# Performance work log

Hardware: AMD Instinct MI355X
Metric: run time of the kernel (lower is better)

Reference implementation:

```python
import jax, jax.numpy as jnp
import numpy as np

NEG_BIG = -9.0e15  # matches -9000000000000000.0 in the torch source


def setup_inputs() -> dict:
    key = jax.random.key(0)
    k1, k2 = jax.random.split(key)
    N, D, L = 8192, 128, 2
    features = jax.random.normal(k1, (N, D), dtype=jnp.float32)
    adj_lst = jax.random.randint(k2, (L, N, N), 0, 2, dtype=jnp.int32)
    return {"features": features, "adj_lst": adj_lst}


def reference(features, adj_lst):
    # features: [N, D] float; adj_lst: [L, N, N] int (0/1)
    n_node = features.shape[0]
    for i in range(adj_lst.shape[0]):  # small fixed number of propagation steps
        adj = adj_lst[i]
        mask = adj > 0
        # raw_weight = ones -> masked logits are 1.0 on edges, -9e15 elsewhere
        logits = jnp.where(mask, jnp.float32(1.0), jnp.float32(NEG_BIG))
        attention = jax.nn.softmax(logits, axis=1)          # [N, N] row-stochastic
        prop_fea = attention @ features                     # [N, D] neighbor mean
        adj_num = jnp.sum(adj, axis=1)                      # degree per node
        adj_mask = (adj_num > 0).astype(features.dtype)[:, None]  # [N, 1]
        features = adj_mask * prop_fea + (1.0 - adj_mask) * features
    return features
```

## Files before the change

kernel.cpp:

```cpp
#include <hip/hip_runtime.h>
#include <hip/hip_bf16.h>

typedef __bf16 bf16x8 __attribute__((ext_vector_type(8)));
typedef float f32x4 __attribute__((ext_vector_type(4)));
typedef float f32x16 __attribute__((ext_vector_type(16)));
typedef int int4v __attribute__((ext_vector_type(4)));
typedef unsigned int uint4v __attribute__((ext_vector_type(4)));
typedef unsigned short u16x8 __attribute__((ext_vector_type(8)));

#define N_NODES 8192
#define D_FEAT 128


__device__ __forceinline__ bf16x8 unpack_byte(unsigned dword, int sh) {
  unsigned P = ((dword >> sh) & 0xFFu) * 0x8001u;
  uint4v c;
  c[0] = (P & 0x10001u) * 0x3F80u;
  c[1] = ((P >> 2) & 0x10001u) * 0x3F80u;
  c[2] = ((P >> 4) & 0x10001u) * 0x3F80u;
  c[3] = ((P >> 6) & 0x10001u) * 0x3F80u;
  return __builtin_bit_cast(bf16x8, c);
}

__device__ __forceinline__ void bpk32_store(const float* __restrict__ src,
                                            unsigned short* __restrict__ Bpk,
                                            int W) {
  const int kk = W >> 8;
  const int ng = (W >> 6) & 3;
  const int l = W & 63;
  const int d = ng * 32 + (l & 31);
  const int p0 = kk * 16 + (l >> 5) * 8;
  const int n0 = (p0 >> 8) * 256 + ((p0 >> 3) & 7) * 32 + ((p0 >> 6) & 3);
  u16x8 pk;
#pragma unroll
  for (int e = 0; e < 8; ++e) {
    __bf16 v = (__bf16)src[(long)(n0 + 4 * e) * D_FEAT + d];
    pk[e] = __builtin_bit_cast(unsigned short, v);
  }
  *(u16x8*)(Bpk + (long)W * 8) = pk;
}

__global__ __launch_bounds__(256) void bpk_build32_kernel(
    const float* __restrict__ src, unsigned short* __restrict__ Bpk) {
  bpk32_store(src, Bpk, blockIdx.x * 256 + threadIdx.x);
}

__global__ __launch_bounds__(512, 2) void fused_layer_kernel(
    const int* __restrict__ adj, const unsigned short* __restrict__ Bpk,
    const float* __restrict__ fin, float* __restrict__ fout) {
  __shared__ unsigned bitsL[2][320];
  __shared__ int degL[32];
  __shared__ __align__(16) f32x4 red[4][4][64];

  const int tid = threadIdx.x;
  const int lane = tid & 63;
  const int w = tid >> 6;
  const int ng = w & 3;
  const int kh2 = w >> 2;
  const int l31 = lane & 31;
  const int lh = lane >> 5;
  const int lh8 = lh * 8;
  const int m0 = blockIdx.x * 32;

  const int4v* aB0 = (const int4v*)(adj + ((long)(m0 + w) << 13)) + lane;
  const int4v* aB1 = (const int4v*)(adj + ((long)(m0 + 8 + w) << 13)) + lane;
  const int4v* aB2 = (const int4v*)(adj + ((long)(m0 + 16 + w) << 13)) + lane;
  const int4v* aB3 = (const int4v*)(adj + ((long)(m0 + 24 + w) << 13)) + lane;

  int cnt0 = 0, cnt1 = 0, cnt2 = 0, cnt3 = 0;

#define DO_BALLOT(R0, R1, R2, R3, BUF)                                       \
  {                                                                          \
    const int e_ = lane >> 1;                                                \
    _Pragma("unroll") for (int i = 0; i < 4; ++i) {                          \
      int4v vv = (i == 0) ? (R0) : (i == 1) ? (R1) : (i == 2) ? (R2) : (R3); \
      unsigned long long b0 = __ballot(vv[0] != 0);                          \
      unsigned long long b1 = __ballot(vv[1] != 0);                          \
      unsigned long long b2 = __ballot(vv[2] != 0);                          \
      unsigned long long b3 = __ballot(vv[3] != 0);                          \
      int pc = __popcll(b0) + __popcll(b1) + __popcll(b2) + __popcll(b3);    \
      if (i == 0) cnt0 += pc;                                                \
      if (i == 1) cnt1 += pc;                                                \
      if (i == 2) cnt2 += pc;                                                \
      if (i == 3) cnt3 += pc;                                                \
      unsigned long long bsel = b0;                                          \
      if (e_ == 1) bsel = b1;                                                \
      if (e_ == 2) bsel = b2;                                                \
      if (e_ == 3) bsel = b3;                                                \
      unsigned dv = (lane & 1) ? (unsigned)(bsel >> 32) : (unsigned)bsel;    \
      if (lane < 8) bitsL[BUF][(i * 8 + w) * 10 + lane] = dv;                \
    }                                                                        \
  }

  f32x16 acc = {0.f, 0.f, 0.f, 0.f, 0.f, 0.f, 0.f, 0.f,
                0.f, 0.f, 0.f, 0.f, 0.f, 0.f, 0.f, 0.f};

#define DO_GEMM(C, BUF)                                                      \
  {                                                                          \
    const bf16x8* bp = (const bf16x8*)Bpk +                                  \
                       (((long)((C)*16 + kh2 * 8)) << 8) + ng * 64 + lane;   \
    bf16x8 bv0 = bp[0], bv1 = bp[256], bv2 = bp[512], bv3 = bp[768];         \
    bf16x8 bv4 = bp[1024], bv5 = bp[1280], bv6 = bp[1536], bv7 = bp[1792];   \
    const unsigned* bl = &bitsL[BUF][l31 * 10 + kh2 * 4];                    \
    unsigned q0 = bl[0], q1 = bl[1], q2 = bl[2], q3 = bl[3];                 \
    acc = __builtin_amdgcn_mfma_f32_32x32x16_bf16(unpack_byte(q0, lh8),      \
                                                  bv0, acc, 0, 0, 0);        \
    acc = __builtin_amdgcn_mfma_f32_32x32x16_bf16(unpack_byte(q0, lh8 + 16), \
                                                  bv1, acc, 0, 0, 0);        \
    acc = __builtin_amdgcn_mfma_f32_32x32x16_bf16(unpack_byte(q1, lh8),      \
                                                  bv2, acc, 0, 0, 0);        \
    acc = __builtin_amdgcn_mfma_f32_32x32x16_bf16(unpack_byte(q1, lh8 + 16), \
                                                  bv3, acc, 0, 0, 0);        \
    acc = __builtin_amdgcn_mfma_f32_32x32x16_bf16(unpack_byte(q2, lh8),      \
                                                  bv4, acc, 0, 0, 0);        \
    acc = __builtin_amdgcn_mfma_f32_32x32x16_bf16(unpack_byte(q2, lh8 + 16), \
                                                  bv5, acc, 0, 0, 0);        \
    acc = __builtin_amdgcn_mfma_f32_32x32x16_bf16(unpack_byte(q3, lh8),      \
                                                  bv6, acc, 0, 0, 0);        \
    acc = __builtin_amdgcn_mfma_f32_32x32x16_bf16(unpack_byte(q3, lh8 + 16), \
                                                  bv7, acc, 0, 0, 0);        \
  }

  int4v avA0 = aB0[0], avA1 = aB1[0], avA2 = aB2[0], avA3 = aB3[0];
  int4v avB0 = aB0[64], avB1 = aB1[64], avB2 = aB2[64], avB3 = aB3[64];
  DO_BALLOT(avA0, avA1, avA2, avA3, 0)
  __syncthreads();

#define BODY(C, CUR0, CUR1, CUR2, CUR3, OTH0, OTH1, OTH2, OTH3)              \
  {                                                                          \
    if ((C) + 2 < 32) {                                                      \
      CUR0 = aB0[((C) + 2) * 64];                                            \
      CUR1 = aB1[((C) + 2) * 64];                                            \
      CUR2 = aB2[((C) + 2) * 64];                                            \
      CUR3 = aB3[((C) + 2) * 64];                                            \
    }                                                                        \
    if ((C) + 1 < 32) DO_BALLOT(OTH0, OTH1, OTH2, OTH3, ((C) + 1) & 1)       \
    DO_GEMM((C), (C)&1)                                                      \
    __syncthreads();                                                         \
  }

  for (int c = 0; c < 32; c += 2) {
    BODY(c, avA0, avA1, avA2, avA3, avB0, avB1, avB2, avB3)
    BODY(c + 1, avB0, avB1, avB2, avB3, avA0, avA1, avA2, avA3)
  }
#undef BODY
#undef DO_GEMM
#undef DO_BALLOT

  if (lane == 0) {
    degL[w] = cnt0;
    degL[8 + w] = cnt1;
    degL[16 + w] = cnt2;
    degL[24 + w] = cnt3;
  }

  if (kh2) {
#define ST4(c)                                                               \
  red[ng][c][lane] = __builtin_shufflevector(acc, acc, 4 * (c), 4 * (c) + 1, \
                                             4 * (c) + 2, 4 * (c) + 3);
    ST4(0) ST4(1) ST4(2) ST4(3)
#undef ST4
  }
  __syncthreads();
  if (kh2) return;
#pragma unroll
  for (int c = 0; c < 4; ++c) {
    f32x4 r = red[ng][c][lane];
#pragma unroll
    for (int k = 0; k < 4; ++k) acc[4 * c + k] += r[k];
  }

#pragma unroll
  for (int r = 0; r < 16; ++r) {
    const int row32 = (r & 3) + 8 * (r >> 2) + 4 * lh;
    const int row = m0 + row32;
    const int dg = degL[row32];
    const long off = (long)row * D_FEAT + ng * 32 + l31;
    fout[off] = dg > 0 ? acc[r] * (1.0f / (float)dg) : fin[off];
  }
}

__global__ __launch_bounds__(256) void transpose_cast_kernel(
    const float* __restrict__ src, unsigned short* __restrict__ dst) {
  __shared__ float tile[64][129];
  const int t = threadIdx.x;
  const int nbase = blockIdx.x * 64;
#pragma unroll
  for (int i = 0; i < 32; ++i) {
    int idx = t + i * 256;
    int nl = idx >> 7;
    int d = idx & 127;
    tile[nl][d] = src[(long)(nbase + nl) * D_FEAT + d];
  }
  __syncthreads();
#pragma unroll
  for (int i = 0; i < 32; ++i) {
    int idx = t + i * 256;
    int d = idx >> 6;
    int nl = idx & 63;
    __bf16 b = (__bf16)tile[nl][d];
    dst[(long)d * N_NODES + nbase + nl] = __builtin_bit_cast(unsigned short, b);
  }
}

__global__ __launch_bounds__(512) void layer_kernel_direct(
    const int* __restrict__ adj, const unsigned short* __restrict__ BT,
    const float* __restrict__ fin, float* __restrict__ fout) {
  const int tid = threadIdx.x;
  const int lane = tid & 63;
  const int w = tid >> 6;
  const int m0 = blockIdx.x * 32 + (w >> 2) * 16;
  const int n0 = (w & 3) * 32;
  const int lr = lane & 15;
  const int kc = lane >> 4;

  const int4v* ap = (const int4v*)(adj + (long)(m0 + lr) * N_NODES + kc * 8);
  const bf16x8* bp0 = (const bf16x8*)(BT + (long)(n0 + lr) * N_NODES + kc * 8);
  const bf16x8* bp1 =
      (const bf16x8*)(BT + (long)(n0 + 16 + lr) * N_NODES + kc * 8);

  f32x4 acc0 = {0.f, 0.f, 0.f, 0.f};
  f32x4 acc1 = {0.f, 0.f, 0.f, 0.f};
  int degv = 0;

#pragma unroll 4
  for (int k = 0; k < N_NODES; k += 32) {
    int4v alo = ap[0];
    int4v ahi = ap[1];
    bf16x8 b0 = bp0[0];
    bf16x8 b1 = bp1[0];
    ap += 8;
    bp0 += 4;
    bp1 += 4;
    unsigned short u[8];
    u[0] = alo[0] ? 0x3F80 : 0;
    u[1] = alo[1] ? 0x3F80 : 0;
    u[2] = alo[2] ? 0x3F80 : 0;
    u[3] = alo[3] ? 0x3F80 : 0;
    u[4] = ahi[0] ? 0x3F80 : 0;
    u[5] = ahi[1] ? 0x3F80 : 0;
    u[6] = ahi[2] ? 0x3F80 : 0;
    u[7] = ahi[3] ? 0x3F80 : 0;
    degv += alo[0] + alo[1] + alo[2] + alo[3] + ahi[0] + ahi[1] + ahi[2] +
            ahi[3];
    bf16x8 a;
    memcpy(&a, u, 16);
    acc0 = __builtin_amdgcn_mfma_f32_16x16x32_bf16(a, b0, acc0, 0, 0, 0);
    acc1 = __builtin_amdgcn_mfma_f32_16x16x32_bf16(a, b1, acc1, 0, 0, 0);
  }

  degv += __shfl_xor(degv, 16);
  degv += __shfl_xor(degv, 32);
  int dgv[4];
#pragma unroll
  for (int j = 0; j < 4; ++j) dgv[j] = __shfl(degv, kc * 4 + j);

#pragma unroll
  for (int t = 0; t < 2; ++t) {
    const f32x4 acc = t ? acc1 : acc0;
    const int col = n0 + t * 16 + lr;
#pragma unroll
    for (int j = 0; j < 4; ++j) {
      const long off = (long)(m0 + kc * 4 + j) * D_FEAT + col;
      fout[off] = dgv[j] > 0 ? acc[j] * (1.0f / (float)dgv[j]) : fin[off];
    }
  }
}

extern "C" void kernel_launch(void* const* d_in, const int* in_sizes, int n_in,
                              void* d_out, int out_size, void* d_ws,
                              size_t ws_size, hipStream_t stream) {
  const float* features = (const float*)d_in[0];
  const int* adj = (const int*)d_in[1];
  float* out = (float*)d_out;
  const long NN = (long)N_NODES * N_NODES;

  const size_t BPK_BYTES = (size_t)D_FEAT * N_NODES * 2;
  const size_t NEED = BPK_BYTES + 256;

  if (ws_size >= NEED) {
    unsigned short* Bpk = (unsigned short*)d_ws;

    bpk_build32_kernel<<<512, 256, 0, stream>>>(features, Bpk);
    fused_layer_kernel<<<256, 512, 0, stream>>>(adj, Bpk, features, out);
    bpk_build32_kernel<<<512, 256, 0, stream>>>(out, Bpk);
    fused_layer_kernel<<<256, 512, 0, stream>>>(adj + NN, Bpk, out, out);
  } else {
    unsigned short* BTw = (unsigned short*)d_ws;
    transpose_cast_kernel<<<N_NODES / 64, 256, 0, stream>>>(features, BTw);
    layer_kernel_direct<<<N_NODES / 32, 512, 0, stream>>>(adj, BTw, features,
                                                          out);
    transpose_cast_kernel<<<N_NODES / 64, 256, 0, stream>>>(out, BTw);
    layer_kernel_direct<<<N_NODES / 32, 512, 0, stream>>>(adj + NN, BTw, out,
                                                          out);
  }
}
```

Baseline: 157.6 us.

## Split-K adjacency GEMM with 128-row tiles, XCD-aware mapping, and combine pass

Each layer's main kernel now handles a 128-row by quarter-K tile instead of 32 rows over the full K. Each wave processes 16 adjacency rows and computes two 32x32 accumulators, so each loaded B fragment feeds two MFMAs. Block indices are remapped so blocks on the same XCD share a K quarter, which should improve L2 reuse of the packed features. Partial sums and degrees go to workspace and a new combine kernel reduces them, adding extra global traffic, a launch per layer and a larger workspace requirement.

```diff
diff --git a/kernel.cpp b/kernel.cpp
--- a/kernel.cpp
+++ b/kernel.cpp
@@ -45,139 +45,151 @@
   bpk32_store(src, Bpk, blockIdx.x * 256 + threadIdx.x);
 }
 
-__global__ __launch_bounds__(512, 2) void fused_layer_kernel(
+__global__ __launch_bounds__(512, 2) void fused_split_kernel(
     const int* __restrict__ adj, const unsigned short* __restrict__ Bpk,
-    const float* __restrict__ fin, float* __restrict__ fout) {
-  __shared__ unsigned bitsL[2][320];
-  __shared__ int degL[32];
-  __shared__ __align__(16) f32x4 red[4][4][64];
+    float* __restrict__ pC, unsigned short* __restrict__ degP) {
+  __shared__ unsigned bitsL[2][1536];
 
   const int tid = threadIdx.x;
   const int lane = tid & 63;
   const int w = tid >> 6;
-  const int ng = w & 3;
-  const int kh2 = w >> 2;
   const int l31 = lane & 31;
   const int lh = lane >> 5;
   const int lh8 = lh * 8;
-  const int m0 = blockIdx.x * 32;
-
-  const int4v* aB0 = (const int4v*)(adj + ((long)(m0 + w) << 13)) + lane;
-  const int4v* aB1 = (const int4v*)(adj + ((long)(m0 + 8 + w) << 13)) + lane;
-  const int4v* aB2 = (const int4v*)(adj + ((long)(m0 + 16 + w) << 13)) + lane;
-  const int4v* aB3 = (const int4v*)(adj + ((long)(m0 + 24 + w) << 13)) + lane;
-
-  int cnt0 = 0, cnt1 = 0, cnt2 = 0, cnt3 = 0;
-
-#define DO_BALLOT(R0, R1, R2, R3, BUF)                                       \
+  const int mh = w >> 2;
+  const int ng = w & 3;
+
+  const int bx = blockIdx.x;
+  const int xcd = bx & 7;
+  const int kq = xcd >> 1;
+  const int rowblk = (bx >> 3) + ((xcd & 1) << 5);
+  const int m0 = rowblk * 128;
+
+  const int* aR = adj + ((long)(m0 + w * 16) << 13) + (long)kq * 2048;
+
+  int4v av[16];
+  int cnt[16];
+#pragma unroll
+  for (int i = 0; i < 16; ++i) cnt[i] = 0;
+
+  f32x16 accA = {0.f, 0.f, 0.f, 0.f, 0.f, 0.f, 0.f, 0.f,
+                 0.f, 0.f, 0.f, 0.f, 0.f, 0.f, 0.f, 0.f};
+  f32x16 accB = accA;
+
+#define LOAD_CHUNK(C)                                                        \
+  {                                                                          \
+    _Pragma("unroll") for (int i = 0; i < 16; ++i)                           \
+        av[i] = *((const int4v*)(aR + ((long)i << 13)) + (C)*64 + lane);     \
+  }
+
+#define DO_BALLOT(BUF)                                                       \
   {                                                                          \
     const int e_ = lane >> 1;                                                \
-    _Pragma("unroll") for (int i = 0; i < 4; ++i) {                          \
-      int4v vv = (i == 0) ? (R0) : (i == 1) ? (R1) : (i == 2) ? (R2) : (R3); \
-      unsigned long long b0 = __ballot(vv[0] != 0);                          \
-      unsigned long long b1 = __ballot(vv[1] != 0);                          \
-      unsigned long long b2 = __ballot(vv[2] != 0);                          \
-      unsigned long long b3 = __ballot(vv[3] != 0);                          \
-      int pc = __popcll(b0) + __popcll(b1) + __popcll(b2) + __popcll(b3);    \
-      if (i == 0) cnt0 += pc;                                                \
-      if (i == 1) cnt1 += pc;                                                \
-      if (i == 2) cnt2 += pc;                                                \
-      if (i == 3) cnt3 += pc;                                                \
+    _Pragma("unroll") for (int i = 0; i < 16; ++i) {                         \
+      unsigned long long b0 = __ballot(av[i][0] != 0);                       \
+      unsigned long long b1 = __ballot(av[i][1] != 0);                       \
+      unsigned long long b2 = __ballot(av[i][2] != 0);                       \
+      unsigned long long b3 = __ballot(av[i][3] != 0);                       \
+      cnt[i] += __popcll(b0) + __popcll(b1) + __popcll(b2) + __popcll(b3);   \
       unsigned long long bsel = b0;                                          \
       if (e_ == 1) bsel = b1;                                                \
       if (e_ == 2) bsel = b2;                                                \
       if (e_ == 3) bsel = b3;                                                \
       unsigned dv = (lane & 1) ? (unsigned)(bsel >> 32) : (unsigned)bsel;    \
-      if (lane < 8) bitsL[BUF][(i * 8 + w) * 10 + lane] = dv;                \
+      if (lane < 8) bitsL[BUF][(w * 16 + i) * 12 + lane] = dv;               \
     }                                                                        \
   }
 
-  f32x16 acc = {0.f, 0.f, 0.f, 0.f, 0.f, 0.f, 0.f, 0.f,
-                0.f, 0.f, 0.f, 0.f, 0.f, 0.f, 0.f, 0.f};
-
-#define DO_GEMM(C, BUF)                                                      \
+#define GEMM_HALF(C, BUF, KH2)                                               \
   {                                                                          \
     const bf16x8* bp = (const bf16x8*)Bpk +                                  \
-                       (((long)((C)*16 + kh2 * 8)) << 8) + ng * 64 + lane;   \
+        (((long)((kq * 8 + (C)) * 16 + (KH2)*8)) << 8) + ng * 64 + lane;     \
     bf16x8 bv0 = bp[0], bv1 = bp[256], bv2 = bp[512], bv3 = bp[768];         \
     bf16x8 bv4 = bp[1024], bv5 = bp[1280], bv6 = bp[1536], bv7 = bp[1792];   \
-    const unsigned* bl = &bitsL[BUF][l31 * 10 + kh2 * 4];                    \
-    unsigned q0 = bl[0], q1 = bl[1], q2 = bl[2], q3 = bl[3];                 \
-    acc = __builtin_amdgcn_mfma_f32_32x32x16_bf16(unpack_byte(q0, lh8),      \
-                                                  bv0, acc, 0, 0, 0);        \
-    acc = __builtin_amdgcn_mfma_f32_32x32x16_bf16(unpack_byte(q0, lh8 + 16), \
-                                                  bv1, acc, 0, 0, 0);        \
-    acc = __builtin_amdgcn_mfma_f32_32x32x16_bf16(unpack_byte(q1, lh8),      \
-                                                  bv2, acc, 0, 0, 0);        \
-    acc = __builtin_amdgcn_mfma_f32_32x32x16_bf16(unpack_byte(q1, lh8 + 16), \
-                                                  bv3, acc, 0, 0, 0);        \
-    acc = __builtin_amdgcn_mfma_f32_32x32x16_bf16(unpack_byte(q2, lh8),      \
-                                                  bv4, acc, 0, 0, 0);        \
-    acc = __builtin_amdgcn_mfma_f32_32x32x16_bf16(unpack_byte(q2, lh8 + 16), \
-                                                  bv5, acc, 0, 0, 0);        \
-    acc = __builtin_amdgcn_mfma_f32_32x32x16_bf16(unpack_byte(q3, lh8),      \
-                                                  bv6, acc, 0, 0, 0);        \
-    acc = __builtin_amdgcn_mfma_f32_32x32x16_bf16(unpack_byte(q3, lh8 + 16), \
-                                                  bv7, acc, 0, 0, 0);        \
-  }
-
-  int4v avA0 = aB0[0], avA1 = aB1[0], avA2 = aB2[0], avA3 = aB3[0];
-  int4v avB0 = aB0[64], avB1 = aB1[64], avB2 = aB2[64], avB3 = aB3[64];
-  DO_BALLOT(avA0, avA1, avA2, avA3, 0)
+    const uint4v* bq = (const uint4v*)(&bitsL[BUF][0]);                      \
+    uint4v qA = bq[(mh * 64 + l31) * 3 + (KH2)];                             \
+    uint4v qB = bq[(mh * 64 + 32 + l31) * 3 + (KH2)];                        \
+    accA = __builtin_amdgcn_mfma_f32_32x32x16_bf16(unpack_byte(qA[0], lh8),  \
+                                                   bv0, accA, 0, 0, 0);      \
+    accB = __builtin_amdgcn_mfma_f32_32x32x16_bf16(unpack_byte(qB[0], lh8),  \
+                                                   bv0, accB, 0, 0, 0);      \
+    accA = __builtin_amdgcn_mfma_f32_32x32x16_bf16(                          \
+        unpack_byte(qA[0], lh8 + 16), bv1, accA, 0, 0, 0);                   \
+    accB = __builtin_amdgcn_mfma_f32_32x32x16_bf16(                          \
+        unpack_byte(qB[0], lh8 + 16), bv1, accB, 0, 0, 0);                   \
+    accA = __builtin_amdgcn_mfma_f32_32x32x16_bf16(unpack_byte(qA[1], lh8),  \
+                                                   bv2, accA, 0, 0, 0);      \
+    accB = __builtin_amdgcn_mfma_f32_32x32x16_bf16(unpack_byte(qB[1], lh8),  \
+                                                   bv2, accB, 0, 0, 0);      \
+    accA = __builtin_amdgcn_mfma_f32_32x32x16_bf16(                          \
+        unpack_byte(qA[1], lh8 + 16), bv3, accA, 0, 0, 0);                   \
+    accB = __builtin_amdgcn_mfma_f32_32x32x16_bf16(                          \
+        unpack_byte(qB[1], lh8 + 16), bv3, accB, 0, 0, 0);                   \
+    accA = __builtin_amdgcn_mfma_f32_32x32x16_bf16(unpack_byte(qA[2], lh8),  \
+                                                   bv4, accA, 0, 0, 0);      \
+    accB = __builtin_amdgcn_mfma_f32_32x32x16_bf16(unpack_byte(qB[2], lh8),  \
+                                                   bv4, accB, 0, 0, 0);      \
+    accA = __builtin_amdgcn_mfma_f32_32x32x16_bf16(                          \
+        unpack_byte(qA[2], lh8 + 16), bv5, accA, 0, 0, 0);                   \
+    accB = __builtin_amdgcn_mfma_f32_32x32x16_bf16(                          \
+        unpack_byte(qB[2], lh8 + 16), bv5, accB, 0, 0, 0);                   \
+    accA = __builtin_amdgcn_mfma_f32_32x32x16_bf16(unpack_byte(qA[3], lh8),  \
+                                                   bv6, accA, 0, 0, 0);      \
+    accB = __builtin_amdgcn_mfma_f32_32x32x16_bf16(unpack_byte(qB[3], lh8),  \
+                                                   bv6, accB, 0, 0, 0);      \
+    accA = __builtin_amdgcn_mfma_f32_32x32x16_bf16(                          \
+        unpack_byte(qA[3], lh8 + 16), bv7, accA, 0, 0, 0);                   \
+    accB = __builtin_amdgcn_mfma_f32_32x32x16_bf16(                          \
+        unpack_byte(qB[3], lh8 + 16), bv7, accB, 0, 0, 0);                   \
+  }
+
+  LOAD_CHUNK(0)
+  DO_BALLOT(0)
+  LOAD_CHUNK(1)
   __syncthreads();
 
-#define BODY(C, CUR0, CUR1, CUR2, CUR3, OTH0, OTH1, OTH2, OTH3)              \
-  {                                                                          \
-    if ((C) + 2 < 32) {                                                      \
-      CUR0 = aB0[((C) + 2) * 64];                                            \
-      CUR1 = aB1[((C) + 2) * 64];                                            \
-      CUR2 = aB2[((C) + 2) * 64];                                            \
-      CUR3 = aB3[((C) + 2) * 64];                                            \
-    }                                                                        \
-    if ((C) + 1 < 32) DO_BALLOT(OTH0, OTH1, OTH2, OTH3, ((C) + 1) & 1)       \
-    DO_GEMM((C), (C)&1)                                                      \
-    __syncthreads();                                                         \
-  }
-
-  for (int c = 0; c < 32; c += 2) {
-    BODY(c, avA0, avA1, avA2, avA3, avB0, avB1, avB2, avB3)
-    BODY(c + 1, avB0, avB1, avB2, avB3, avA0, avA1, avA2, avA3)
-  }
-#undef BODY
-#undef DO_GEMM
+  for (int c = 0; c < 8; ++c) {
+    if (c + 1 < 8) DO_BALLOT((c + 1) & 1)
+    if (c + 2 < 8) LOAD_CHUNK(c + 2)
+    GEMM_HALF(c, c & 1, 0)
+    GEMM_HALF(c, c & 1, 1)
+    __syncthreads();
+  }
+#undef GEMM_HALF
 #undef DO_BALLOT
+#undef LOAD_CHUNK
 
   if (lane == 0) {
-    degL[w] = cnt0;
-    degL[8 + w] = cnt1;
-    degL[16 + w] = cnt2;
-    degL[24 + w] = cnt3;
-  }
-
-  if (kh2) {
-#define ST4(c)                                                               \
-  red[ng][c][lane] = __builtin_shufflevector(acc, acc, 4 * (c), 4 * (c) + 1, \
-                                             4 * (c) + 2, 4 * (c) + 3);
-    ST4(0) ST4(1) ST4(2) ST4(3)
-#undef ST4
-  }
-  __syncthreads();
-  if (kh2) return;
-#pragma unroll
-  for (int c = 0; c < 4; ++c) {
-    f32x4 r = red[ng][c][lane];
-#pragma unroll
-    for (int k = 0; k < 4; ++k) acc[4 * c + k] += r[k];
-  }
-
+#pragma unroll
+    for (int i = 0; i < 16; ++i)
+      degP[kq * N_NODES + m0 + w * 16 + i] = (unsigned short)cnt[i];
+  }
+
+  float* base = pC + ((long)kq << 20);
 #pragma unroll
   for (int r = 0; r < 16; ++r) {
-    const int row32 = (r & 3) + 8 * (r >> 2) + 4 * lh;
-    const int row = m0 + row32;
-    const int dg = degL[row32];
-    const long off = (long)row * D_FEAT + ng * 32 + l31;
-    fout[off] = dg > 0 ? acc[r] * (1.0f / (float)dg) : fin[off];
-  }
+    const int rr = (r & 3) + 8 * (r >> 2) + 4 * lh;
+    base[(long)(m0 + mh * 64 + rr) * D_FEAT + ng * 32 + l31] = accA[r];
+    base[(long)(m0 + mh * 64 + 32 + rr) * D_FEAT + ng * 32 + l31] = accB[r];
+  }
+}
+
+__global__ __launch_bounds__(256) void combine_kernel(
+    const float* __restrict__ pC, const unsigned short* __restrict__ degP,
+    const float* __restrict__ fin, float* __restrict__ fout) {
+  const int g = blockIdx.x * 256 + threadIdx.x;
+  const int row = g >> 5;
+  const f32x4* P = (const f32x4*)pC;
+  f32x4 s = P[g] + P[262144 + g] + P[524288 + g] + P[786432 + g];
+  const int dg = (int)degP[row] + degP[N_NODES + row] + degP[2 * N_NODES + row] +
+                 degP[3 * N_NODES + row];
+  f32x4 o;
+  if (dg > 0) {
+    o = s * (1.0f / (float)dg);
+  } else {
+    o = ((const f32x4*)fin)[g];
+  }
+  ((f32x4*)fout)[g] = o;
 }
 
 __global__ __launch_bounds__(256) void transpose_cast_kernel(
@@ -275,16 +287,23 @@
   float* out = (float*)d_out;
   const long NN = (long)N_NODES * N_NODES;
 
+  const size_t PC_BYTES = 4ul * N_NODES * D_FEAT * 4;
+  const size_t DEG_BYTES = 4ul * N_NODES * 2;
   const size_t BPK_BYTES = (size_t)D_FEAT * N_NODES * 2;
-  const size_t NEED = BPK_BYTES + 256;
+  const size_t NEED = PC_BYTES + DEG_BYTES + BPK_BYTES;
 
   if (ws_size >= NEED) {
-    unsigned short* Bpk = (unsigned short*)d_ws;
+    float* pC = (float*)d_ws;
+    unsigned short* degP = (unsigned short*)((char*)d_ws + PC_BYTES);
+    unsigned short* Bpk =
+        (unsigned short*)((char*)d_ws + PC_BYTES + DEG_BYTES);
 
     bpk_build32_kernel<<<512, 256, 0, stream>>>(features, Bpk);
-    fused_layer_kernel<<<256, 512, 0, stream>>>(adj, Bpk, features, out);
+    fused_split_kernel<<<256, 512, 0, stream>>>(adj, Bpk, pC, degP);
+    combine_kernel<<<1024, 256, 0, stream>>>(pC, degP, features, out);
     bpk_build32_kernel<<<512, 256, 0, stream>>>(out, Bpk);
-    fused_layer_kernel<<<256, 512, 0, stream>>>(adj + NN, Bpk, out, out);
+    fused_split_kernel<<<256, 512, 0, stream>>>(adj + NN, Bpk, pC, degP);
+    combine_kernel<<<1024, 256, 0, stream>>>(pC, degP, out, out);
   } else {
     unsigned short* BTw = (unsigned short*)d_ws;
     transpose_cast_kernel<<<N_NODES / 64, 256, 0, stream>>>(features, BTw);
```

Result: slower. 171.7 us (+9.0%).

## Split the reduction dimension across two blocks and add a combine kernel

Applied to the files above, without the earlier changes.

Each layer's fused kernel now runs 512 blocks, and each block handles half of the K (neighbor) range for a 32-row tile. The partial sums and partial degree counts go to workspace, and a new combine kernel adds them, normalizes by degree, or falls back to the input features. The goal is more blocks than the 256-CU device so the memory-bound adjacency stream keeps more CUs busy. The cost is an extra kernel launch per layer, plus the traffic to write and reread the partial results.

```diff
diff --git a/kernel.cpp b/kernel.cpp
--- a/kernel.cpp
+++ b/kernel.cpp
@@ -45,11 +45,10 @@
   bpk32_store(src, Bpk, blockIdx.x * 256 + threadIdx.x);
 }
 
-__global__ __launch_bounds__(512, 2) void fused_layer_kernel(
+__global__ __launch_bounds__(512, 2) void fused_split2_kernel(
     const int* __restrict__ adj, const unsigned short* __restrict__ Bpk,
-    const float* __restrict__ fin, float* __restrict__ fout) {
+    float* __restrict__ pC, unsigned short* __restrict__ degP) {
   __shared__ unsigned bitsL[2][320];
-  __shared__ int degL[32];
   __shared__ __align__(16) f32x4 red[4][4][64];
 
   const int tid = threadIdx.x;
@@ -60,12 +59,20 @@
   const int l31 = lane & 31;
   const int lh = lane >> 5;
   const int lh8 = lh * 8;
-  const int m0 = blockIdx.x * 32;
-
-  const int4v* aB0 = (const int4v*)(adj + ((long)(m0 + w) << 13)) + lane;
-  const int4v* aB1 = (const int4v*)(adj + ((long)(m0 + 8 + w) << 13)) + lane;
-  const int4v* aB2 = (const int4v*)(adj + ((long)(m0 + 16 + w) << 13)) + lane;
-  const int4v* aB3 = (const int4v*)(adj + ((long)(m0 + 24 + w) << 13)) + lane;
+
+  const int bx = blockIdx.x;
+  const int rowblk = bx >> 1;
+  const int kh = bx & 1;
+  const int m0 = rowblk * 32;
+
+  const int4v* aB0 =
+      (const int4v*)(adj + ((long)(m0 + w) << 13) + kh * 4096) + lane;
+  const int4v* aB1 =
+      (const int4v*)(adj + ((long)(m0 + 8 + w) << 13) + kh * 4096) + lane;
+  const int4v* aB2 =
+      (const int4v*)(adj + ((long)(m0 + 16 + w) << 13) + kh * 4096) + lane;
+  const int4v* aB3 =
+      (const int4v*)(adj + ((long)(m0 + 24 + w) << 13) + kh * 4096) + lane;
 
   int cnt0 = 0, cnt1 = 0, cnt2 = 0, cnt3 = 0;
 
@@ -97,8 +104,9 @@
 
 #define DO_GEMM(C, BUF)                                                      \
   {                                                                          \
-    const bf16x8* bp = (const bf16x8*)Bpk +                                  \
-                       (((long)((C)*16 + kh2 * 8)) << 8) + ng * 64 + lane;   \
+    const bf16x8* bp =                                                       \
+        (const bf16x8*)Bpk +                                                 \
+        (((long)(kh * 256 + (C)*16 + kh2 * 8)) << 8) + ng * 64 + lane;       \
     bf16x8 bv0 = bp[0], bv1 = bp[256], bv2 = bp[512], bv3 = bp[768];         \
     bf16x8 bv4 = bp[1024], bv5 = bp[1280], bv6 = bp[1536], bv7 = bp[1792];   \
     const unsigned* bl = &bitsL[BUF][l31 * 10 + kh2 * 4];                    \
@@ -128,18 +136,18 @@
 
 #define BODY(C, CUR0, CUR1, CUR2, CUR3, OTH0, OTH1, OTH2, OTH3)              \
   {                                                                          \
-    if ((C) + 2 < 32) {                                                      \
+    if ((C) + 2 < 16) {                                                      \
       CUR0 = aB0[((C) + 2) * 64];                                            \
       CUR1 = aB1[((C) + 2) * 64];                                            \
       CUR2 = aB2[((C) + 2) * 64];                                            \
       CUR3 = aB3[((C) + 2) * 64];                                            \
     }                                                                        \
-    if ((C) + 1 < 32) DO_BALLOT(OTH0, OTH1, OTH2, OTH3, ((C) + 1) & 1)       \
+    if ((C) + 1 < 16) DO_BALLOT(OTH0, OTH1, OTH2, OTH3, ((C) + 1) & 1)       \
     DO_GEMM((C), (C)&1)                                                      \
     __syncthreads();                                                         \
   }
 
-  for (int c = 0; c < 32; c += 2) {
+  for (int c = 0; c < 16; c += 2) {
     BODY(c, avA0, avA1, avA2, avA3, avB0, avB1, avB2, avB3)
     BODY(c + 1, avB0, avB1, avB2, avB3, avA0, avA1, avA2, avA3)
   }
@@ -148,10 +156,11 @@
 #undef DO_BALLOT
 
   if (lane == 0) {
-    degL[w] = cnt0;
-    degL[8 + w] = cnt1;
-    degL[16 + w] = cnt2;
-    degL[24 + w] = cnt3;
+    unsigned short* dp = degP + kh * N_NODES + m0;
+    dp[w] = (unsigned short)cnt0;
+    dp[8 + w] = (unsigned short)cnt1;
+    dp[16 + w] = (unsigned short)cnt2;
+    dp[24 + w] = (unsigned short)cnt3;
   }
 
   if (kh2) {
@@ -170,14 +179,29 @@
     for (int k = 0; k < 4; ++k) acc[4 * c + k] += r[k];
   }
 
+  float* base = pC + (long)kh * N_NODES * D_FEAT;
 #pragma unroll
   for (int r = 0; r < 16; ++r) {
     const int row32 = (r & 3) + 8 * (r >> 2) + 4 * lh;
-    const int row = m0 + row32;
-    const int dg = degL[row32];
-    const long off = (long)row * D_FEAT + ng * 32 + l31;
-    fout[off] = dg > 0 ? acc[r] * (1.0f / (float)dg) : fin[off];
-  }
+    base[(long)(m0 + row32) * D_FEAT + ng * 32 + l31] = acc[r];
+  }
+}
+
+__global__ __launch_bounds__(256) void combine2_kernel(
+    const float* __restrict__ pC, const unsigned short* __restrict__ degP,
+    const float* __restrict__ fin, float* __restrict__ fout) {
+  const int g = blockIdx.x * 256 + threadIdx.x;
+  const int row = g >> 5;
+  const f32x4* P = (const f32x4*)pC;
+  f32x4 s = P[g] + P[262144 + g];
+  const int dg = (int)degP[row] + (int)degP[N_NODES + row];
+  f32x4 o;
+  if (dg > 0) {
+    o = s * (1.0f / (float)dg);
+  } else {
+    o = ((const f32x4*)fin)[g];
+  }
+  ((f32x4*)fout)[g] = o;
 }
 
 __global__ __launch_bounds__(256) void transpose_cast_kernel(
@@ -275,16 +299,23 @@
   float* out = (float*)d_out;
   const long NN = (long)N_NODES * N_NODES;
 
+  const size_t PC_BYTES = 2ul * N_NODES * D_FEAT * 4;
+  const size_t DEG_BYTES = 2ul * N_NODES * 2;
   const size_t BPK_BYTES = (size_t)D_FEAT * N_NODES * 2;
-  const size_t NEED = BPK_BYTES + 256;
+  const size_t NEED = PC_BYTES + DEG_BYTES + BPK_BYTES;
 
   if (ws_size >= NEED) {
-    unsigned short* Bpk = (unsigned short*)d_ws;
+    float* pC = (float*)d_ws;
+    unsigned short* degP = (unsigned short*)((char*)d_ws + PC_BYTES);
+    unsigned short* Bpk =
+        (unsigned short*)((char*)d_ws + PC_BYTES + DEG_BYTES);
 
     bpk_build32_kernel<<<512, 256, 0, stream>>>(features, Bpk);
-    fused_layer_kernel<<<256, 512, 0, stream>>>(adj, Bpk, features, out);
+    fused_split2_kernel<<<512, 512, 0, stream>>>(adj, Bpk, pC, degP);
+    combine2_kernel<<<1024, 256, 0, stream>>>(pC, degP, features, out);
     bpk_build32_kernel<<<512, 256, 0, stream>>>(out, Bpk);
-    fused_layer_kernel<<<256, 512, 0, stream>>>(adj + NN, Bpk, out, out);
+    fused_split2_kernel<<<512, 512, 0, stream>>>(adj + NN, Bpk, pC, degP);
+    combine2_kernel<<<1024, 256, 0, stream>>>(pC, degP, out, out);
   } else {
     unsigned short* BTw = (unsigned short*)d_ws;
     transpose_cast_kernel<<<N_NODES / 64, 256, 0, stream>>>(features, BTw);
```

Result: slower. 164.9 us (+4.6%).

## Split adjacency bitmask build and MFMA GEMM into two separate phases

Applied to the files above, without the earlier changes.

Instead of interleaving the adjacency ballot with the GEMM chunk by chunk under a barrier each step, the kernel first streams the whole 32-row adjacency slab into a full shared-memory bitmask. Degrees are accumulated with shared atomics during this pass. It then runs the MFMA loop over all 32 K-chunks with double-buffered B register loads and no barriers. This removes 32 block-wide syncs and gives the HBM adjacency stream simple coalesced loads, at the cost of about 40KB of shared memory and no overlap between adjacency reading and matrix math.

```diff
diff --git a/kernel.cpp b/kernel.cpp
--- a/kernel.cpp
+++ b/kernel.cpp
@@ -48,7 +48,7 @@
 __global__ __launch_bounds__(512, 2) void fused_layer_kernel(
     const int* __restrict__ adj, const unsigned short* __restrict__ Bpk,
     const float* __restrict__ fin, float* __restrict__ fout) {
-  __shared__ unsigned bitsL[2][320];
+  __shared__ unsigned bitsF[32][320];
   __shared__ int degL[32];
   __shared__ __align__(16) f32x4 red[4][4][64];
 
@@ -61,98 +61,96 @@
   const int lh = lane >> 5;
   const int lh8 = lh * 8;
   const int m0 = blockIdx.x * 32;
-
-  const int4v* aB0 = (const int4v*)(adj + ((long)(m0 + w) << 13)) + lane;
-  const int4v* aB1 = (const int4v*)(adj + ((long)(m0 + 8 + w) << 13)) + lane;
-  const int4v* aB2 = (const int4v*)(adj + ((long)(m0 + 16 + w) << 13)) + lane;
-  const int4v* aB3 = (const int4v*)(adj + ((long)(m0 + 24 + w) << 13)) + lane;
-
-  int cnt0 = 0, cnt1 = 0, cnt2 = 0, cnt3 = 0;
-
-#define DO_BALLOT(R0, R1, R2, R3, BUF)                                       \
+  const int e_ = lane >> 1;
+
+  if (tid < 32) degL[tid] = 0;
+  __syncthreads();
+
+  const int4v* ap = (const int4v*)(adj + ((long)m0 << 13)) + tid;
+
+#define BALLOT_ONE(V, I, PC)                                                 \
   {                                                                          \
-    const int e_ = lane >> 1;                                                \
-    _Pragma("unroll") for (int i = 0; i < 4; ++i) {                          \
-      int4v vv = (i == 0) ? (R0) : (i == 1) ? (R1) : (i == 2) ? (R2) : (R3); \
-      unsigned long long b0 = __ballot(vv[0] != 0);                          \
-      unsigned long long b1 = __ballot(vv[1] != 0);                          \
-      unsigned long long b2 = __ballot(vv[2] != 0);                          \
-      unsigned long long b3 = __ballot(vv[3] != 0);                          \
-      int pc = __popcll(b0) + __popcll(b1) + __popcll(b2) + __popcll(b3);    \
-      if (i == 0) cnt0 += pc;                                                \
-      if (i == 1) cnt1 += pc;                                                \
-      if (i == 2) cnt2 += pc;                                                \
-      if (i == 3) cnt3 += pc;                                                \
-      unsigned long long bsel = b0;                                          \
-      if (e_ == 1) bsel = b1;                                                \
-      if (e_ == 2) bsel = b2;                                                \
-      if (e_ == 3) bsel = b3;                                                \
-      unsigned dv = (lane & 1) ? (unsigned)(bsel >> 32) : (unsigned)bsel;    \
-      if (lane < 8) bitsL[BUF][(i * 8 + w) * 10 + lane] = dv;                \
-    }                                                                        \
-  }
+    unsigned long long b0 = __ballot((V)[0] != 0);                           \
+    unsigned long long b1 = __ballot((V)[1] != 0);                           \
+    unsigned long long b2 = __ballot((V)[2] != 0);                           \
+    unsigned long long b3 = __ballot((V)[3] != 0);                           \
+    PC += __popcll(b0) + __popcll(b1) + __popcll(b2) + __popcll(b3);         \
+    unsigned long long bsel = b0;                                            \
+    if (e_ == 1) bsel = b1;                                                  \
+    if (e_ == 2) bsel = b2;                                                  \
+    if (e_ == 3) bsel = b3;                                                  \
+    unsigned dv = (lane & 1) ? (unsigned)(bsel >> 32) : (unsigned)bsel;      \
+    if (lane < 8)                                                            \
+      bitsF[((((I)) & 3) << 3) + w][(((I)) >> 2) * 10 + lane] = dv;          \
+  }
+
+  {
+    int4v va = ap[0];
+    int4v vb = ap[512];
+    int4v vc = ap[1024];
+    int4v vd = ap[1536];
+    for (int i = 0; i < 128; i += 4) {
+      int pc = 0;
+      BALLOT_ONE(va, i, pc)
+      if (i + 4 < 128) va = ap[(i + 4) * 512];
+      BALLOT_ONE(vb, i + 1, pc)
+      if (i + 5 < 128) vb = ap[(i + 5) * 512];
+      BALLOT_ONE(vc, i + 2, pc)
+      if (i + 6 < 128) vc = ap[(i + 6) * 512];
+      BALLOT_ONE(vd, i + 3, pc)
+      if (i + 7 < 128) vd = ap[(i + 7) * 512];
+      if (lane == 0) atomicAdd(&degL[i >> 2], pc);
+    }
+  }
+#undef BALLOT_ONE
+  __syncthreads();
 
   f32x16 acc = {0.f, 0.f, 0.f, 0.f, 0.f, 0.f, 0.f, 0.f,
                 0.f, 0.f, 0.f, 0.f, 0.f, 0.f, 0.f, 0.f};
 
-#define DO_GEMM(C, BUF)                                                      \
+  const bf16x8* bpb =
+      (const bf16x8*)Bpk + ((kh2 * 8) << 8) + ng * 64 + lane;
+
+#define LOADB(BUF, C)                                                        \
   {                                                                          \
-    const bf16x8* bp = (const bf16x8*)Bpk +                                  \
-                       (((long)((C)*16 + kh2 * 8)) << 8) + ng * 64 + lane;   \
-    bf16x8 bv0 = bp[0], bv1 = bp[256], bv2 = bp[512], bv3 = bp[768];         \
-    bf16x8 bv4 = bp[1024], bv5 = bp[1280], bv6 = bp[1536], bv7 = bp[1792];   \
-    const unsigned* bl = &bitsL[BUF][l31 * 10 + kh2 * 4];                    \
+    _Pragma("unroll") for (int j = 0; j < 8; ++j)                            \
+        BUF[j] = bpb[(long)(C)*4096 + j * 256];                              \
+  }
+
+#define COMPUTE(C, BUF)                                                      \
+  {                                                                          \
+    const unsigned* bl = &bitsF[(C)][l31 * 10 + kh2 * 4];                    \
     unsigned q0 = bl[0], q1 = bl[1], q2 = bl[2], q3 = bl[3];                 \
     acc = __builtin_amdgcn_mfma_f32_32x32x16_bf16(unpack_byte(q0, lh8),      \
-                                                  bv0, acc, 0, 0, 0);        \
+                                                  BUF[0], acc, 0, 0, 0);     \
     acc = __builtin_amdgcn_mfma_f32_32x32x16_bf16(unpack_byte(q0, lh8 + 16), \
-                                                  bv1, acc, 0, 0, 0);        \
+                                                  BUF[1], acc, 0, 0, 0);     \
     acc = __builtin_amdgcn_mfma_f32_32x32x16_bf16(unpack_byte(q1, lh8),      \
-                                                  bv2, acc, 0, 0, 0);        \
+                                                  BUF[2], acc, 0, 0, 0);     \
     acc = __builtin_amdgcn_mfma_f32_32x32x16_bf16(unpack_byte(q1, lh8 + 16), \
-                                                  bv3, acc, 0, 0, 0);        \
+                                                  BUF[3], acc, 0, 0, 0);     \
     acc = __builtin_amdgcn_mfma_f32_32x32x16_bf16(unpack_byte(q2, lh8),      \
-                                                  bv4, acc, 0, 0, 0);        \
+                                                  BUF[4], acc, 0, 0, 0);     \
     acc = __builtin_amdgcn_mfma_f32_32x32x16_bf16(unpack_byte(q2, lh8 + 16), \
-                                                  bv5, acc, 0, 0, 0);        \
+                                                  BUF[5], acc, 0, 0, 0);     \
     acc = __builtin_amdgcn_mfma_f32_32x32x16_bf16(unpack_byte(q3, lh8),      \
-                                                  bv6, acc, 0, 0, 0);        \
+                                                  BUF[6], acc, 0, 0, 0);     \
     acc = __builtin_amdgcn_mfma_f32_32x32x16_bf16(unpack_byte(q3, lh8 + 16), \
-                                                  bv7, acc, 0, 0, 0);        \
-  }
-
-  int4v avA0 = aB0[0], avA1 = aB1[0], avA2 = aB2[0], avA3 = aB3[0];
-  int4v avB0 = aB0[64], avB1 = aB1[64], avB2 = aB2[64], avB3 = aB3[64];
-  DO_BALLOT(avA0, avA1, avA2, avA3, 0)
-  __syncthreads();
-
-#define BODY(C, CUR0, CUR1, CUR2, CUR3, OTH0, OTH1, OTH2, OTH3)              \
-  {                                                                          \
-    if ((C) + 2 < 32) {                                                      \
-      CUR0 = aB0[((C) + 2) * 64];                                            \
-      CUR1 = aB1[((C) + 2) * 64];                                            \
-      CUR2 = aB2[((C) + 2) * 64];                                            \
-      CUR3 = aB3[((C) + 2) * 64];                                            \
-    }                                                                        \
-    if ((C) + 1 < 32) DO_BALLOT(OTH0, OTH1, OTH2, OTH3, ((C) + 1) & 1)       \
-    DO_GEMM((C), (C)&1)                                                      \
-    __syncthreads();                                                         \
-  }
-
-  for (int c = 0; c < 32; c += 2) {
-    BODY(c, avA0, avA1, avA2, avA3, avB0, avB1, avB2, avB3)
-    BODY(c + 1, avB0, avB1, avB2, avB3, avA0, avA1, avA2, avA3)
-  }
-#undef BODY
-#undef DO_GEMM
-#undef DO_BALLOT
-
-  if (lane == 0) {
-    degL[w] = cnt0;
-    degL[8 + w] = cnt1;
-    degL[16 + w] = cnt2;
-    degL[24 + w] = cnt3;
-  }
+                                                  BUF[7], acc, 0, 0, 0);     \
+  }
+
+  {
+    bf16x8 bA[8], bB[8];
+    LOADB(bA, 0)
+    for (int c = 0; c < 32; c += 2) {
+      LOADB(bB, c + 1)
+      COMPUTE(c, bA)
+      if (c + 2 < 32) LOADB(bA, c + 2)
+      COMPUTE(c + 1, bB)
+    }
+  }
+#undef COMPUTE
+#undef LOADB
 
   if (kh2) {
 #define ST4(c)                                                               \
```

Result: faster. 149.9 us, median of 2 (-4.9%).
